# Performance work log

Hardware: AMD Instinct MI355X
Metric: run time of the kernel (lower is better)

## Reference

```python
import jax, jax.numpy as jnp
import numpy as np

B, S, D = 4, 2048, 1024
H, DH = 16, 64  # dim_q = dim_k = D // H
DFF = 4096


def setup_inputs() -> dict:
    key = jax.random.key(0)
    ks = jax.random.split(key, 12)
    sd = 0.02
    x = jax.random.normal(ks[0], (B, S, D), dtype=jnp.float32)
    mask = jax.random.randint(ks[1], (B, S, S), 0, 2) == 1  # True = masked
    Wq = jax.random.normal(ks[2], (H, D, DH), dtype=jnp.float32) * sd
    bq = jnp.zeros((H, DH), dtype=jnp.float32)
    Wk = jax.random.normal(ks[3], (H, D, DH), dtype=jnp.float32) * sd
    bk = jnp.zeros((H, DH), dtype=jnp.float32)
    Wv = jax.random.normal(ks[4], (H, D, DH), dtype=jnp.float32) * sd
    bv = jnp.zeros((H, DH), dtype=jnp.float32)
    Wo = jax.random.normal(ks[5], (H * DH, D), dtype=jnp.float32) * sd
    bo = jnp.zeros((D,), dtype=jnp.float32)
    W1 = jax.random.normal(ks[6], (D, DFF), dtype=jnp.float32) * sd
    b1 = jnp.zeros((DFF,), dtype=jnp.float32)
    W2 = jax.random.normal(ks[7], (DFF, D), dtype=jnp.float32) * sd
    b2 = jnp.zeros((D,), dtype=jnp.float32)
    return dict(x=x, mask=mask, Wq=Wq, bq=bq, Wk=Wk, bk=bk, Wv=Wv, bv=bv,
                Wo=Wo, bo=bo, W1=W1, b1=b1, W2=W2, b2=b2)


def reference(x, mask, Wq, bq, Wk, bk, Wv, bv, Wo, bo, W1, b1, W2, b2):
    # x: [B,S,D]; mask: [B,S,S] bool (True -> masked)
    # Per-head projections, batched over heads: [B,H,S,DH]
    q = jnp.einsum('bsd,hde->bhse', x, Wq) + bq[None, :, None, :]
    k = jnp.einsum('bsd,hde->bhse', x, Wk) + bk[None, :, None, :]
    v = jnp.einsum('bsd,hde->bhse', x, Wv) + bv[None, :, None, :]
    # NOTE: source scales by sqrt(seq_len) (query.size(1)), reproduced faithfully.
    scale = x.shape[1] ** 0.5
    scores = jnp.einsum('bhse,bhte->bhst', q, k) / scale  # [B,H,S,S]
    scores = jnp.where(mask[:, None, :, :], -1e9, scores)
    attn = jax.nn.softmax(scores, axis=-1)
    ctx = jnp.einsum('bhst,bhte->bhse', attn, v)  # [B,H,S,DH]
    # concat heads -> [B,S,H*DH], output projection
    ctx = jnp.transpose(ctx, (0, 2, 1, 3)).reshape(x.shape[0], x.shape[1], -1)
    out = ctx @ Wo + bo
    # FFN (no residual/LayerNorm in source; dropout = identity in eval)
    h = jax.nn.relu(out @ W1 + b1)
    return h @ W2 + b2
```

## Files before the change

kernel.cpp:

```cpp
#include <hip/hip_runtime.h>
#include <hip/hip_bf16.h>


#define SDIM 2048
#define DDIM 1024

using floatx4 = __attribute__((ext_vector_type(4))) float;
using bf16x8  = __attribute__((ext_vector_type(8))) __bf16;
using bf16x4  = __attribute__((ext_vector_type(4))) __bf16;
using short4v = __attribute__((ext_vector_type(4))) short;

#define GLDS16(gptr, lptr)                                                        \
    __builtin_amdgcn_global_load_lds(                                             \
        (const __attribute__((address_space(1))) void*)(uintptr_t)(gptr),         \
        (__attribute__((address_space(3))) void*)(uintptr_t)(lptr), 16, 0, 0)


__global__ void k_f2b(const float* __restrict__ in, __bf16* __restrict__ out) {
    long i = ((long)blockIdx.x * 256 + threadIdx.x) * 4;
    float4 f = *(const float4*)(in + i);
    bf16x4 v;
    v[0] = (__bf16)f.x; v[1] = (__bf16)f.y; v[2] = (__bf16)f.z; v[3] = (__bf16)f.w;
    *(bf16x4*)(out + i) = v;
}

__global__ void k_tr(const float* __restrict__ in, __bf16* __restrict__ out, int R, int C) {
    __shared__ float t[32][33];
    int nrt = R >> 5;
    int tr = blockIdx.x % nrt, tc = blockIdx.x / nrt;
    int r0 = tr * 32, c0 = tc * 32;
    int lx = threadIdx.x & 31, ly = threadIdx.x >> 5;
    #pragma unroll
    for (int i = 0; i < 32; i += 8) t[ly + i][lx] = in[(long)(r0 + ly + i) * C + c0 + lx];
    __syncthreads();
    #pragma unroll
    for (int i = 0; i < 32; i += 8) out[(long)(c0 + ly + i) * R + r0 + lx] = (__bf16)t[lx][ly + i];
}

__global__ void k_pack_qkvw(const float* __restrict__ Wq, const float* __restrict__ Wk,
                            const float* __restrict__ Wv, __bf16* __restrict__ out) {
    int bid = blockIdx.x;
    int dht = bid & 1;
    int dt = (bid >> 1) & 31;
    int h = (bid >> 6) & 15;
    int which = bid >> 10;
    const float* W = (which == 0) ? Wq : (which == 1) ? Wk : Wv;
    __shared__ float t[32][33];
    int lx = threadIdx.x & 31, ly = threadIdx.x >> 5;
    const float* src = W + ((long)h * 1024 + dt * 32) * 64 + dht * 32;
    #pragma unroll
    for (int i = 0; i < 32; i += 8) t[ly + i][lx] = src[(ly + i) * 64 + lx];
    __syncthreads();
    __bf16* dst = out + ((long)(which * 1024 + h * 64 + dht * 32)) * 1024 + dt * 32;
    #pragma unroll
    for (int i = 0; i < 32; i += 8) dst[(long)(ly + i) * 1024 + lx] = (__bf16)t[lx][ly + i];
}

__global__ void k_pack_qkvb(const float* bq, const float* bk, const float* bv, float* out) {
    int i = blockIdx.x * 256 + threadIdx.x;
    if (i < 3072) {
        int which = i >> 10, r = i & 1023;
        const float* s = (which == 0) ? bq : (which == 1) ? bk : bv;
        out[i] = s[r];
    }
}

__global__ void k_probe(const unsigned* __restrict__ m, int* flag) {
    __shared__ int bad;
    if (threadIdx.x == 0) bad = 0;
    __syncthreads();
    int local = 0;
    for (int i = 0; i < 64; i++) {
        unsigned w = m[threadIdx.x + 256 * i];
        if (w != 0u && w != 1u && w != 0x3f800000u) local = 1;
    }
    if (local) atomicOr(&bad, 1);
    __syncthreads();
    if (threadIdx.x == 0) *flag = bad ? 0 : 1;
}

__global__ void k_pack_mask(const void* __restrict__ mask, const int* __restrict__ flag,
                            unsigned long long* __restrict__ bits) {
    long wid = ((long)blockIdx.x * 256 + threadIdx.x) >> 6;
    int lane = threadIdx.x & 63;
    long e = wid * 64 + lane;
    bool pred;
    if (*flag) pred = ((const unsigned*)mask)[e] != 0u;
    else       pred = ((const unsigned char*)mask)[e] != 0;
    unsigned long long bal = __ballot(pred);
    if (lane == 0) bits[wid] = bal;
}

__global__ void k_remap(const unsigned* __restrict__ bitsDW, unsigned* __restrict__ out) {
    int t = blockIdx.x * 256 + threadIdx.x;
    int q = t & 3, kt = (t >> 2) & 15, srow = t >> 6;
    uint4 md = *(const uint4*)(bitsDW + (long)srow * 64 + kt * 4);
    unsigned d[4] = {md.x, md.y, md.z, md.w};
    unsigned acc = 0;
    #pragma unroll
    for (int ct = 0; ct < 8; ct++) {
        unsigned nib = (d[ct >> 1] >> (((ct & 1) << 4) + q * 4)) & 0xFu;
        acc |= nib << (ct * 4);
    }
    out[srow * 64 + q * 16 + kt] = acc;
}

__global__ void k_trv(const __bf16* __restrict__ Vrow, __bf16* __restrict__ Vt) {
    __shared__ __bf16 t[32][72];
    int p = blockIdx.x >> 6, ts = blockIdx.x & 63;
    int tid = threadIdx.x;
    const __bf16* src = Vrow + ((long)p * 2048 + ts * 32) * 64;
    int s = tid >> 3, c = (tid & 7) * 8;
    *(bf16x8*)&t[s][c] = *(const bf16x8*)&src[s * 64 + c];
    __syncthreads();
    int dh = tid >> 2, sb = (tid & 3) * 8;
    bf16x8 w;
    #pragma unroll
    for (int j = 0; j < 8; j++) w[j] = t[sb + j][dh];
    *(bf16x8*)&Vt[((long)p * 64 + dh) * 2048 + ts * 32 + sb] = w;
}

#define QSZ 8388608L

template <int MODE>
__global__ __launch_bounds__(256, 4) void k_gemm(const __bf16* __restrict__ A,
                                                 const __bf16* __restrict__ Bt,
                                                 const float* __restrict__ bias,
                                                 void* __restrict__ Cout, int Ndim, int K) {
    __shared__ __align__(16) __bf16 As[128 * 64];
    __shared__ __align__(16) __bf16 Bs[128 * 64];
    const int tid = threadIdx.x;
    const int wave = tid >> 6, lane = tid & 63;
    const int q = lane >> 4, l16 = lane & 15;
    const int wr = wave >> 1, wc = wave & 1;
    const long bm = (long)blockIdx.x * 128;
    const long bn = (long)blockIdx.y * 128;
    floatx4 acc[4][4] = {};

    const int srow = lane >> 3;
    const int scol = (((lane & 7) - srow) & 7) * 8;
    const int r8 = l16 & 7;

    const char* apA0 = (const char*)As + (wr * 64 + l16) * 128 + ((q + r8) & 7) * 16;
    const char* apA1 = (const char*)As + (wr * 64 + l16) * 128 + ((q + 4 + r8) & 7) * 16;
    const char* apB0 = (const char*)Bs + (wc * 64 + l16) * 128 + ((q + r8) & 7) * 16;
    const char* apB1 = (const char*)Bs + (wc * 64 + l16) * 128 + ((q + 4 + r8) & 7) * 16;

    for (int k0 = 0; k0 < K; k0 += 64) {
        __syncthreads();
        #pragma unroll
        for (int c = 0; c < 4; c++) {
            int row0 = wave * 32 + c * 8;
            GLDS16(&A[(bm + row0 + srow) * K + k0 + scol], (char*)As + row0 * 128);
            GLDS16(&Bt[(bn + row0 + srow) * K + k0 + scol], (char*)Bs + row0 * 128);
        }
        __syncthreads();
        bf16x8 af[4], bfr[4];
        #pragma unroll
        for (int i = 0; i < 4; i++) af[i] = *(const bf16x8*)(apA0 + i * 2048);
        #pragma unroll
        for (int j = 0; j < 4; j++) bfr[j] = *(const bf16x8*)(apB0 + j * 2048);
        #pragma unroll
        for (int i = 0; i < 4; i++)
            #pragma unroll
            for (int j = 0; j < 4; j++)
                acc[i][j] = __builtin_amdgcn_mfma_f32_16x16x32_bf16(af[i], bfr[j], acc[i][j], 0, 0, 0);
        #pragma unroll
        for (int i = 0; i < 4; i++) af[i] = *(const bf16x8*)(apA1 + i * 2048);
        #pragma unroll
        for (int j = 0; j < 4; j++) bfr[j] = *(const bf16x8*)(apB1 + j * 2048);
        #pragma unroll
        for (int i = 0; i < 4; i++)
            #pragma unroll
            for (int j = 0; j < 4; j++)
                acc[i][j] = __builtin_amdgcn_mfma_f32_16x16x32_bf16(af[i], bfr[j], acc[i][j], 0, 0, 0);
    }

    const int mrow0 = (int)bm + wr * 64 + q * 4;
    const int ncol0 = (int)bn + wc * 64;
    #pragma unroll
    for (int j = 0; j < 4; j++) {
        int nbase = ncol0 + j * 16 + l16;
        float bv = bias[nbase];
        #pragma unroll
        for (int i = 0; i < 4; i++) {
            #pragma unroll
            for (int r = 0; r < 4; r++) {
                int mm = mrow0 + i * 16 + r;
                float v = acc[i][j][r] + bv;
                if (MODE == 2) v = fmaxf(v, 0.f);
                if (MODE == 3) {
                    ((float*)Cout)[(long)mm * Ndim + nbase] = v;
                } else if (MODE == 0) {
                    int which = nbase >> 10, rem = nbase & 1023;
                    int hh = rem >> 6, dh = rem & 63;
                    int bb = mm >> 11, ss = mm & 2047;
                    long pr = (long)(bb * 16 + hh);
                    __bf16* o = (__bf16*)Cout;
                    if (which == 0) {
                        v *= 0.03188152837f;
                        o[(pr * 2048 + ss) * 64 + dh] = (__bf16)v;
                    } else if (which == 1) o[QSZ + (pr * 2048 + ss) * 64 + dh] = (__bf16)v;
                    else o[3 * QSZ + (pr * 2048 + ss) * 64 + dh] = (__bf16)v;
                } else {
                    ((__bf16*)Cout)[(long)mm * Ndim + nbase] = (__bf16)v;
                }
            }
        }
    }
}

__global__ __launch_bounds__(256, 2) void k_attn(const __bf16* __restrict__ Q,
                                                 const __bf16* __restrict__ Kb,
                                                 const __bf16* __restrict__ Vt,
                                                 const unsigned* __restrict__ bitw2,
                                                 __bf16* __restrict__ ctx) {
    __shared__ __align__(16) __bf16 Qs[128 * 64];
    __shared__ __align__(16) __bf16 Ks[2][128 * 64];
    __shared__ __align__(16) __bf16 Vts[2][64 * 128];
    const int tid = threadIdx.x, wave = tid >> 6, lane = tid & 63;
    const int q = lane >> 4, l16 = lane & 15;
    const int pair = blockIdx.x & 63, qt = blockIdx.x >> 6;
    const int b = pair >> 4, h = pair & 15;

    const int srow8 = lane >> 3;
    const int scol8 = (((lane & 7) - srow8) & 7) * 8;
    const int r8 = l16 & 7;
    const int vrow = lane >> 4;
    const int vl = lane & 15;

    const char* kp0 = (const char*)Ks + l16 * 128 + ((q + r8) & 7) * 16;
    const char* kp1 = (const char*)Ks + l16 * 128 + ((q + 4 + r8) & 7) * 16;
    const char* vp[8];
    #pragma unroll
    for (int ct = 0; ct < 8; ct++)
        vp[ct] = (const char*)Vts + l16 * 256 + (q & 1) * 8 + ((ct * 2 + (q >> 1) + l16) & 15) * 16;
    const int qrow = qt * 128 + wave * 32 + l16;
    const unsigned* mp0 = bitw2 + ((long)(b * SDIM + qrow)) * 64 + q * 16;
    const unsigned* mp1 = mp0 + 16 * 64;

    floatx4 o[2][4] = {};
    floatx4 o5[2] = {};
    short4v ones;
    { union { unsigned u[2]; short4v s; } c; c.u[0] = 0x3F803F80u; c.u[1] = 0x3F803F80u; ones = c.s; }

    auto stage_kv = [&](int kt, int bufsel) __attribute__((always_inline)) {
        const __bf16* Kp = Kb + ((long)pair * SDIM + kt * 128) * 64;
        #pragma unroll
        for (int c = 0; c < 4; c++) {
            int row0 = wave * 32 + c * 8;
            GLDS16(&Kp[(row0 + srow8) * 64 + scol8], (char*)Ks + bufsel * 16384 + row0 * 128);
        }
        const __bf16* Vp = Vt + ((long)pair * 64) * SDIM + kt * 128;
        #pragma unroll
        for (int c = 0; c < 4; c++) {
            int row0 = wave * 16 + c * 4;
            int gsrc = ((vl - (c * 4 + vrow)) & 15) * 8;
            GLDS16(&Vp[(long)(row0 + vrow) * SDIM + gsrc], (char*)Vts + bufsel * 16384 + row0 * 256);
        }
    };

    const __bf16* Qp = Q + ((long)pair * SDIM + qt * 128) * 64;
    #pragma unroll
    for (int c = 0; c < 4; c++) {
        int row0 = wave * 32 + c * 8;
        GLDS16(&Qp[(row0 + srow8) * 64 + scol8], (char*)Qs + row0 * 128);
    }
    unsigned waA = mp0[0], wbA = mp1[0];
    stage_kv(0, 0);
    asm volatile("s_waitcnt vmcnt(8)\n\ts_barrier" ::: "memory");

    bf16x8 qf[2][2];
    #pragma unroll
    for (int g = 0; g < 2; g++) {
        const char* qb = (const char*)Qs + (wave * 32 + g * 16 + l16) * 128;
        qf[g][0] = *(const bf16x8*)(qb + ((q + r8) & 7) * 16);
        qf[g][1] = *(const bf16x8*)(qb + ((q + 4 + r8) & 7) * 16);
    }

    auto compute = [&](int off, unsigned w32a, unsigned w32b) __attribute__((always_inline)) {
        __builtin_amdgcn_s_setprio(1);
        floatx4 st0[8], st1[8];
        #pragma unroll
        for (int ct = 0; ct < 8; ct++) {
            bf16x8 kf0 = *(const bf16x8*)(kp0 + off + ct * 2048);
            bf16x8 kf1 = *(const bf16x8*)(kp1 + off + ct * 2048);
            floatx4 z0 = {}, z1 = {};
            z0 = __builtin_amdgcn_mfma_f32_16x16x32_bf16(kf0, qf[0][0], z0, 0, 0, 0);
            z1 = __builtin_amdgcn_mfma_f32_16x16x32_bf16(kf0, qf[1][0], z1, 0, 0, 0);
            z0 = __builtin_amdgcn_mfma_f32_16x16x32_bf16(kf1, qf[0][1], z0, 0, 0, 0);
            z1 = __builtin_amdgcn_mfma_f32_16x16x32_bf16(kf1, qf[1][1], z1, 0, 0, 0);
            st0[ct] = z0; st1[ct] = z1;
        }
        #pragma unroll
        for (int ct = 0; ct < 8; ct++) {
            union { unsigned u[2]; short4v s; } pu0, pu1;
            {
                float p0 = __builtin_amdgcn_exp2f(st0[ct][0]);
                float p1 = __builtin_amdgcn_exp2f(st0[ct][1]);
                float p2 = __builtin_amdgcn_exp2f(st0[ct][2]);
                float p3 = __builtin_amdgcn_exp2f(st0[ct][3]);
                p0 = (w32a & (1u << (ct * 4 + 0))) ? 0.f : p0;
                p1 = (w32a & (1u << (ct * 4 + 1))) ? 0.f : p1;
                p2 = (w32a & (1u << (ct * 4 + 2))) ? 0.f : p2;
                p3 = (w32a & (1u << (ct * 4 + 3))) ? 0.f : p3;
                union { float f; unsigned u; } c0, c1, c2, c3;
                c0.f = p0; c1.f = p1; c2.f = p2; c3.f = p3;
                pu0.u[0] = __builtin_amdgcn_perm(c1.u, c0.u, 0x07060302u);
                pu0.u[1] = __builtin_amdgcn_perm(c3.u, c2.u, 0x07060302u);
            }
            {
                float p0 = __builtin_amdgcn_exp2f(st1[ct][0]);
                float p1 = __builtin_amdgcn_exp2f(st1[ct][1]);
                float p2 = __builtin_amdgcn_exp2f(st1[ct][2]);
                float p3 = __builtin_amdgcn_exp2f(st1[ct][3]);
                p0 = (w32b & (1u << (ct * 4 + 0))) ? 0.f : p0;
                p1 = (w32b & (1u << (ct * 4 + 1))) ? 0.f : p1;
                p2 = (w32b & (1u << (ct * 4 + 2))) ? 0.f : p2;
                p3 = (w32b & (1u << (ct * 4 + 3))) ? 0.f : p3;
                union { float f; unsigned u; } c0, c1, c2, c3;
                c0.f = p0; c1.f = p1; c2.f = p2; c3.f = p3;
                pu1.u[0] = __builtin_amdgcn_perm(c1.u, c0.u, 0x07060302u);
                pu1.u[1] = __builtin_amdgcn_perm(c3.u, c2.u, 0x07060302u);
            }
            #pragma unroll
            for (int d = 0; d < 4; d++) {
                union { bf16x4 b; short4v s; } vu;
                vu.b = *(const bf16x4*)(vp[ct] + off + d * 4096);
                o[0][d] = __builtin_amdgcn_mfma_f32_16x16x16bf16_1k(vu.s, pu0.s, o[0][d], 0, 0, 0);
                o[1][d] = __builtin_amdgcn_mfma_f32_16x16x16bf16_1k(vu.s, pu1.s, o[1][d], 0, 0, 0);
            }
            o5[0] = __builtin_amdgcn_mfma_f32_16x16x16bf16_1k(ones, pu0.s, o5[0], 0, 0, 0);
            o5[1] = __builtin_amdgcn_mfma_f32_16x16x16bf16_1k(ones, pu1.s, o5[1], 0, 0, 0);
        }
        __builtin_amdgcn_s_setprio(0);
    };

    #pragma unroll 1
    for (int kt = 0; kt < 14; kt += 2) {
        unsigned waB = mp0[kt + 1], wbB = mp1[kt + 1];
        stage_kv(kt + 1, 1);
        asm volatile("s_waitcnt vmcnt(10)\n\ts_barrier" ::: "memory");
        compute(0, waA, wbA);
        asm volatile("s_barrier" ::: "memory");
        waA = mp0[kt + 2]; wbA = mp1[kt + 2];
        stage_kv(kt + 2, 0);
        asm volatile("s_waitcnt vmcnt(10)\n\ts_barrier" ::: "memory");
        compute(16384, waB, wbB);
        asm volatile("s_barrier" ::: "memory");
    }
    {
        unsigned waB = mp0[15], wbB = mp1[15];
        stage_kv(15, 1);
        asm volatile("s_waitcnt vmcnt(10)\n\ts_barrier" ::: "memory");
        compute(0, waA, wbA);
        asm volatile("s_barrier" ::: "memory");
        asm volatile("s_waitcnt vmcnt(0)\n\ts_barrier" ::: "memory");
        compute(16384, waB, wbB);
    }

    #pragma unroll
    for (int g = 0; g < 2; g++) {
        float inv = 1.0f / o5[g][0];
        long base = ((long)b * SDIM + qrow + g * 16) * DDIM + h * 64;
        #pragma unroll
        for (int d = 0; d < 4; d++) {
            bf16x4 w;
            #pragma unroll
            for (int r = 0; r < 4; r++) w[r] = (__bf16)(o[g][d][r] * inv);
            *(bf16x4*)&ctx[base + d * 16 + q * 4] = w;
        }
    }
}


extern "C" void kernel_launch(void* const* d_in, const int* in_sizes, int n_in,
                              void* d_out, int out_size, void* d_ws, size_t ws_size,
                              hipStream_t stream) {
    const float* x = (const float*)d_in[0];
    const void* mask = d_in[1];
    const float* Wq = (const float*)d_in[2];
    const float* bq = (const float*)d_in[3];
    const float* Wk = (const float*)d_in[4];
    const float* bk = (const float*)d_in[5];
    const float* Wv = (const float*)d_in[6];
    const float* bv = (const float*)d_in[7];
    const float* Wo = (const float*)d_in[8];
    const float* bo = (const float*)d_in[9];
    const float* W1 = (const float*)d_in[10];
    const float* b1 = (const float*)d_in[11];
    const float* W2 = (const float*)d_in[12];
    const float* b2 = (const float*)d_in[13];

    char* ws = (char*)d_ws;
    __bf16* xb   = (__bf16*)(ws + 0);
    __bf16* Qb   = (__bf16*)(ws + 16777216);
    __bf16* Kb   = (__bf16*)(ws + 33554432);
    __bf16* Vtb  = (__bf16*)(ws + 50331648);
    __bf16* Vrow = (__bf16*)(ws + 67108864);
    __bf16* hbuf = (__bf16*)(ws + 33554432);
    __bf16* wqkvt = (__bf16*)(ws + 100663296);
    __bf16* wot  = (__bf16*)(ws + 106954752);
    __bf16* w1t  = (__bf16*)(ws + 109051904);
    __bf16* w2t  = (__bf16*)(ws + 117440512);
    float* bqkv  = (float*)(ws + 125829120);
    int* flag    = (int*)(ws + 125841408);
    __bf16* ctx = xb;
    __bf16* attn_out = Qb;
    unsigned long long* bits = (unsigned long long*)wqkvt;
    unsigned* bits2 = (unsigned*)((char*)wqkvt + 2097152);
    (void)Vrow;

    k_f2b<<<8192, 256, 0, stream>>>(x, xb);
    k_pack_qkvw<<<3072, 256, 0, stream>>>(Wq, Wk, Wv, wqkvt);
    k_pack_qkvb<<<12, 256, 0, stream>>>(bq, bk, bv, bqkv);
    k_tr<<<1024, 256, 0, stream>>>(Wo, wot, 1024, 1024);
    k_tr<<<4096, 256, 0, stream>>>(W1, w1t, 1024, 4096);
    k_tr<<<4096, 256, 0, stream>>>(W2, w2t, 4096, 1024);
    k_probe<<<1, 256, 0, stream>>>((const unsigned*)mask, flag);

    {
        dim3 g(64, 24);
        k_gemm<0><<<g, 256, 0, stream>>>(xb, wqkvt, bqkv, (void*)Qb, 3072, 1024);
    }
    k_trv<<<4096, 256, 0, stream>>>(Vrow, Vtb);
    k_pack_mask<<<65536, 256, 0, stream>>>(mask, flag, bits);
    k_remap<<<2048, 256, 0, stream>>>((const unsigned*)bits, bits2);
    k_attn<<<1024, 256, 0, stream>>>(Qb, Kb, Vtb, bits2, ctx);
    {
        dim3 g(64, 8);
        k_gemm<1><<<g, 256, 0, stream>>>(ctx, wot, bo, (void*)attn_out, 1024, 1024);
    }
    {
        dim3 g(64, 32);
        k_gemm<2><<<g, 256, 0, stream>>>(attn_out, w1t, b1, (void*)hbuf, 4096, 1024);
    }
    {
        dim3 g(64, 8);
        k_gemm<3><<<g, 256, 0, stream>>>(hbuf, w2t, b2, d_out, 1024, 4096);
    }
}
```

Before: 592.0 us.

## Stage GEMM epilogue through LDS for coalesced bf16 stores and swizzle block order

The bf16-output GEMM epilogues now write each wave's 64x64 result tile into XOR-swizzled shared memory, then read it back and store 16-byte coalesced rows to global memory. Before, each scattered 2-byte store went straight to global. The work-group index is also remapped with a stride-8 interleave, which changes which tiles run together and is meant to improve L2 reuse of A/B panels. The cost is an extra barrier and an LDS round trip in the epilogue. The fp32 output mode keeps the old direct-store path.

```diff
diff --git a/kernel.cpp b/kernel.cpp
--- a/kernel.cpp
+++ b/kernel.cpp
@@ -133,8 +133,11 @@
     const int wave = tid >> 6, lane = tid & 63;
     const int q = lane >> 4, l16 = lane & 15;
     const int wr = wave >> 1, wc = wave & 1;
-    const long bm = (long)blockIdx.x * 128;
-    const long bn = (long)blockIdx.y * 128;
+    const int nwg = gridDim.x * gridDim.y;
+    const int id = blockIdx.y * gridDim.x + blockIdx.x;
+    const int swz = (id & 7) * (nwg >> 3) + (id >> 3);
+    const long bm = (long)(swz % gridDim.x) * 128;
+    const long bn = (long)(swz / gridDim.x) * 128;
     floatx4 acc[4][4] = {};
 
     const int srow = lane >> 3;
@@ -176,34 +179,66 @@
                 acc[i][j] = __builtin_amdgcn_mfma_f32_16x16x32_bf16(af[i], bfr[j], acc[i][j], 0, 0, 0);
     }
 
-    const int mrow0 = (int)bm + wr * 64 + q * 4;
     const int ncol0 = (int)bn + wc * 64;
-    #pragma unroll
-    for (int j = 0; j < 4; j++) {
-        int nbase = ncol0 + j * 16 + l16;
-        float bv = bias[nbase];
-        #pragma unroll
-        for (int i = 0; i < 4; i++) {
-            #pragma unroll
-            for (int r = 0; r < 4; r++) {
-                int mm = mrow0 + i * 16 + r;
-                float v = acc[i][j][r] + bv;
-                if (MODE == 2) v = fmaxf(v, 0.f);
-                if (MODE == 3) {
+
+    if (MODE != 3) {
+        __syncthreads();
+        char* wbase = (wave < 2) ? ((char*)As + wave * 8192) : ((char*)Bs + (wave - 2) * 8192);
+        const bool qscale = (MODE == 0) && (ncol0 < 1024);
+        #pragma unroll
+        for (int j = 0; j < 4; j++) {
+            float bv = bias[ncol0 + j * 16 + l16];
+            #pragma unroll
+            for (int i = 0; i < 4; i++) {
+                #pragma unroll
+                for (int r = 0; r < 4; r++) {
+                    int lr = q * 4 + i * 16 + r;
+                    int lc = j * 16 + l16;
+                    float v = acc[i][j][r] + bv;
+                    if (MODE == 2) v = fmaxf(v, 0.f);
+                    if (qscale) v *= 0.03188152837f;
+                    *(__bf16*)(wbase + lr * 128 + ((lc * 2) ^ ((lr & 7) << 4))) = (__bf16)v;
+                }
+            }
+        }
+        if (MODE == 0) {
+            const int which = ncol0 >> 10;
+            const int hh = (ncol0 >> 6) & 15;
+            const int rb = (int)bm + wr * 64;
+            const int bb = rb >> 11, ss0 = rb & 2047;
+            const long pr = (long)(bb * 16 + hh);
+            const long dbase = (which == 0) ? 0L : (which == 1) ? QSZ : 3 * QSZ;
+            __bf16* dst = (__bf16*)Cout + dbase + (pr * 2048 + ss0) * 64;
+            #pragma unroll
+            for (int t = 0; t < 8; t++) {
+                int row = t * 8 + (lane >> 3);
+                int chunk = lane & 7;
+                uint4 d = *(const uint4*)(wbase + row * 128 + ((chunk * 16) ^ ((row & 7) << 4)));
+                *(uint4*)((char*)dst + row * 128 + chunk * 16) = d;
+            }
+        } else {
+            __bf16* dst = (__bf16*)Cout + (bm + wr * 64) * Ndim + ncol0;
+            #pragma unroll
+            for (int t = 0; t < 8; t++) {
+                int row = t * 8 + (lane >> 3);
+                int chunk = lane & 7;
+                uint4 d = *(const uint4*)(wbase + row * 128 + ((chunk * 16) ^ ((row & 7) << 4)));
+                *(uint4*)((char*)dst + (long)row * Ndim * 2 + chunk * 16) = d;
+            }
+        }
+    } else {
+        const int mrow0 = (int)bm + wr * 64 + q * 4;
+        #pragma unroll
+        for (int j = 0; j < 4; j++) {
+            int nbase = ncol0 + j * 16 + l16;
+            float bv = bias[nbase];
+            #pragma unroll
+            for (int i = 0; i < 4; i++) {
+                #pragma unroll
+                for (int r = 0; r < 4; r++) {
+                    int mm = mrow0 + i * 16 + r;
+                    float v = acc[i][j][r] + bv;
                     ((float*)Cout)[(long)mm * Ndim + nbase] = v;
-                } else if (MODE == 0) {
-                    int which = nbase >> 10, rem = nbase & 1023;
-                    int hh = rem >> 6, dh = rem & 63;
-                    int bb = mm >> 11, ss = mm & 2047;
-                    long pr = (long)(bb * 16 + hh);
-                    __bf16* o = (__bf16*)Cout;
-                    if (which == 0) {
-                        v *= 0.03188152837f;
-                        o[(pr * 2048 + ss) * 64 + dh] = (__bf16)v;
-                    } else if (which == 1) o[QSZ + (pr * 2048 + ss) * 64 + dh] = (__bf16)v;
-                    else o[3 * QSZ + (pr * 2048 + ss) * 64 + dh] = (__bf16)v;
-                } else {
-                    ((__bf16*)Cout)[(long)mm * Ndim + nbase] = (__bf16)v;
                 }
             }
         }
```

Result: slower. 611.4 us (+3.3%).
